# Kernel tuning notes

Measured on AMD Instinct MI355X. Metric: run time of the kernel, lower is better.

Reference implementation:

```python
import jax, jax.numpy as jnp
import numpy as np

H = 4      # num_heads
C = 64     # attention_num_c
C_Z = 128  # num_in_c (pair rep channels)
C_T = 64   # num_in_c_kv (template pair channels)


def setup_inputs() -> dict:
    key = jax.random.key(0)
    ks = jax.random.split(key, 7)
    B, T, R = 1, 4, 384
    z2d = jax.random.normal(ks[0], (B, R, R, C_Z), dtype=jnp.float32)
    t2d = jax.random.normal(ks[1], (B, T, R, R, C_T), dtype=jnp.float32)
    s = 0.02
    Wq = jax.random.normal(ks[2], (C_Z, H * C), dtype=jnp.float32) * s
    Wk = jax.random.normal(ks[3], (C_T, H * C), dtype=jnp.float32) * s
    Wv = jax.random.normal(ks[4], (C_T, H * C), dtype=jnp.float32) * s
    Wo = jax.random.normal(ks[5], (H * C, C_Z), dtype=jnp.float32) * s
    bo = jax.random.normal(ks[6], (C_Z,), dtype=jnp.float32) * s
    return {"z2d": z2d, "t2d": t2d, "Wq": Wq, "Wk": Wk, "Wv": Wv, "Wo": Wo, "bo": bo}


def reference(z2d, t2d, Wq, Wk, Wv, Wo, bo):
    B, R = z2d.shape[0], z2d.shape[-2]
    T = t2d.shape[1]
    P = R * R  # residue-pair axis
    # query: one query per residue pair
    zq = z2d.reshape(B, P, 1, C_Z)
    # templates become the key/value axis per residue pair
    tkv = jnp.transpose(t2d, (0, 2, 3, 1, 4)).reshape(B, P, T, C_T)
    q = (zq @ Wq).reshape(B, P, 1, H, C) * (C ** -0.5)
    k = (tkv @ Wk).reshape(B, P, T, H, C)
    v = (tkv @ Wv).reshape(B, P, T, H, C)
    logits = jnp.einsum('bpqhc,bpkhc->bphqk', q, k)  # [B,P,H,1,T]
    weights = jax.nn.softmax(logits, axis=-1)
    weighted_avg = jnp.einsum('bphqk,bpkhc->bpqhc', weights, v)  # [B,P,1,H,C]
    out = weighted_avg.reshape(B, P, 1, H * C) @ Wo + bo
    return out.reshape(B, R, R, C_Z)
```

## Files before the change

### kernel.cpp

```cpp
#include <hip/hip_runtime.h>


#define R_    384
#define P_    (R_ * R_)
#define PB    32
#define NPB   256
#define NT_   18

typedef __attribute__((ext_vector_type(8))) short  short8;
typedef __attribute__((ext_vector_type(4))) float  f32x4;

union S8U { short8 s8; unsigned u[4]; };

__device__ __forceinline__ unsigned short f2bf(float f) {
  unsigned u = __float_as_uint(f);
  unsigned r = ((u >> 16) & 1u) + 0x7FFFu;
  return (unsigned short)((u + r) >> 16);
}
__device__ __forceinline__ float bf2f(unsigned short s) {
  return __uint_as_float(((unsigned)s) << 16);
}
__device__ __forceinline__ unsigned cvtpk(float lo, float hi) {
  unsigned d;
  asm("v_cvt_pk_bf16_f32 %0, %1, %2" : "=v"(d) : "v"(lo), "v"(hi));
  return d;
}
__device__ __forceinline__ int swz(int p, int c) {
  return p * 256 + ((((c >> 3) ^ (p & 31)) << 3) | (c & 7));
}
#define SB() __builtin_amdgcn_sched_barrier(0)
#define BAR() do { \
    asm volatile("s_waitcnt lgkmcnt(0)\ns_barrier" ::: "memory"); \
    SB(); \
  } while (0)

__global__ void prep_kernel(const float* __restrict__ Wq, const float* __restrict__ Wk,
                            const float* __restrict__ Wv, const float* __restrict__ Wo,
                            unsigned short* __restrict__ AbarT,
                            unsigned short* __restrict__ MbarT) {
  int tid = blockIdx.x * blockDim.x + threadIdx.x;
  if (tid < 256 * 128) {
    int n = tid >> 7, i = tid & 127;
    int h = n >> 6, j = n & 63;
    const float* wq = Wq + i * 256 + h * 64;
    const float* wk = Wk + j * 256 + h * 64;
    float acc = 0.f;
#pragma unroll 8
    for (int c = 0; c < 64; ++c) acc += wq[c] * wk[c];
    AbarT[n * 128 + i] = f2bf(acc * 0.125f);
  } else {
    int t2 = tid - 256 * 128;
    int o = t2 >> 8, k = t2 & 255;
    int h = k >> 6, j = k & 63;
    const float* wv = Wv + j * 256 + h * 64;
    const float* wo = Wo + (h * 64) * 128 + o;
    float acc = 0.f;
#pragma unroll 8
    for (int c = 0; c < 64; ++c) acc += wv[c] * wo[c * 128];
    MbarT[o * 256 + k] = f2bf(acc);
  }
}

__global__ __launch_bounds__(512, 2) void attn_kernel(
    const float* __restrict__ z2d, const float* __restrict__ t2d,
    const unsigned short* __restrict__ AbarT, const unsigned short* __restrict__ MbarT,
    const float* __restrict__ bo, float* __restrict__ out) {
  extern __shared__ char smem[];
  unsigned short* sAbar = (unsigned short*)smem;
  unsigned short* sG    = (unsigned short*)(smem + 65536);

  const int tid  = threadIdx.x;
  const int wv_  = tid >> 6;
  const int lane = tid & 63;
  const int l = lane & 15;
  const int q = lane >> 4;
  const int mt = wv_ & 1;
  const int ng = wv_ >> 1;

  const int ap = tid >> 4, asub = tid & 15;
  const int ah = asub >> 2, au = asub & 3;
  const int aoG0 = swz(ap, ah * 64 + au * 16);
  const int aoG1 = swz(ap, ah * 64 + au * 16 + 8);

  const int p2g = mt * 16 + l;

#pragma unroll
  for (int k2 = 0; k2 < 8; ++k2) {
    int id = k2 * 512 + tid, n = id >> 4, blk = id & 15;
    short8 v = *(const short8*)(AbarT + n * 128 + blk * 8);
    *(short8*)(sAbar + n * 128 + ((blk ^ (n & 15)) << 3)) = v;
  }
  short8 mb0[8], mb1[8];
#pragma unroll
  for (int kk = 0; kk < 8; ++kk) {
    mb0[kk] = *(const short8*)(MbarT + (size_t)(ng * 32 + l) * 256 + kk * 32 + q * 8);
    mb1[kk] = *(const short8*)(MbarT + (size_t)(ng * 32 + 16 + l) * 256 + kk * 32 + q * 8);
  }
  const float bo0 = bo[ng * 32 + l];
  const float bo1 = bo[ng * 32 + 16 + l];
  SB();
  float4 kt[4][4];
  {
    const float* kb = t2d + ((size_t)blockIdx.x * PB + ap) * 64 + au * 16;
#pragma unroll
    for (int t = 0; t < 4; ++t)
#pragma unroll
      for (int j = 0; j < 4; ++j)
        kt[t][j] = *(const float4*)(kb + (size_t)t * (P_ * 64) + 4 * j);
  }
  SB();
  float4 zb[8];
  {
    const float* zr = z2d + ((size_t)blockIdx.x * PB + mt * 16 + l) * 128;
#pragma unroll
    for (int kk = 0; kk < 4; ++kk) {
      zb[2 * kk]     = *(const float4*)(zr + kk * 32 + q * 8);
      zb[2 * kk + 1] = *(const float4*)(zr + kk * 32 + q * 8 + 4);
    }
  }
  BAR();

#pragma unroll 1
  for (int k = 0; k < NT_; ++k) {
    const int sl = k & 1;
    const size_t P0  = (size_t)(blockIdx.x + (size_t)k * NPB) * PB;
    const size_t P0n = P0 + (size_t)NPB * PB;

    if (k > 0) {
      const unsigned short* sGp = sG + (sl ^ 1) * 8192;
      f32x4 a20 = f32x4{0.f, 0.f, 0.f, 0.f};
      f32x4 a21 = f32x4{0.f, 0.f, 0.f, 0.f};
#pragma unroll
      for (int kk = 0; kk < 8; ++kk) {
        short8 af2 = *(const short8*)(sGp + p2g * 256 + (((kk * 4 + q) ^ p2g) << 3));
        a20 = __builtin_amdgcn_mfma_f32_16x16x32_bf16(af2, mb0[kk], a20, 0, 0, 0);
        a21 = __builtin_amdgcn_mfma_f32_16x16x32_bf16(af2, mb1[kk], a21, 0, 0, 0);
      }
      const size_t rb = (P0 - (size_t)NPB * PB + (size_t)(mt * 16 + q * 4)) * 128;
#pragma unroll
      for (int r = 0; r < 4; ++r) {
        out[rb + r * 128 + ng * 32 + l]      = a20[r] + bo0;
        out[rb + r * 128 + ng * 32 + 16 + l] = a21[r] + bo1;
      }
    }
    SB();
    {
      f32x4 a1[4];
#pragma unroll
      for (int i = 0; i < 4; ++i) a1[i] = f32x4{0.f, 0.f, 0.f, 0.f};
#pragma unroll
      for (int kk = 0; kk < 4; ++kk) {
        S8U af;
        af.u[0] = cvtpk(zb[2 * kk].x,     zb[2 * kk].y);
        af.u[1] = cvtpk(zb[2 * kk].z,     zb[2 * kk].w);
        af.u[2] = cvtpk(zb[2 * kk + 1].x, zb[2 * kk + 1].y);
        af.u[3] = cvtpk(zb[2 * kk + 1].z, zb[2 * kk + 1].w);
#pragma unroll
        for (int i = 0; i < 4; ++i) {
          const int n = (ng * 4 + i) * 16 + l;
          short8 bf = *(const short8*)(sAbar + n * 128 + (((kk * 4 + q) ^ l) << 3));
          a1[i] = __builtin_amdgcn_mfma_f32_16x16x32_bf16(af.s8, bf, a1[i], 0, 0, 0);
        }
      }
      unsigned short* sGc = sG + sl * 8192;
#pragma unroll
      for (int i = 0; i < 4; ++i) {
        const int c = (ng * 4 + i) * 16 + l;
#pragma unroll
        for (int r = 0; r < 4; ++r)
          sGc[swz(mt * 16 + q * 4 + r, c)] = f2bf(a1[i][r]);
      }
    }
    SB();
    if (k + 1 < NT_) {
      const float* zr = z2d + (P0n + (size_t)(mt * 16 + l)) * 128;
#pragma unroll
      for (int kk = 0; kk < 4; ++kk) {
        zb[2 * kk]     = *(const float4*)(zr + kk * 32 + q * 8);
        zb[2 * kk + 1] = *(const float4*)(zr + kk * 32 + q * 8 + 4);
      }
    }
    SB();
    BAR();

    {
      unsigned short* sGc = sG + sl * 8192;
      short8 g0 = *(const short8*)(sGc + aoG0);
      short8 g1 = *(const short8*)(sGc + aoG1);
      float lg0 = 0.f, lg1 = 0.f, lg2 = 0.f, lg3 = 0.f;
#pragma unroll
      for (int j = 0; j < 4; ++j) {
        const float ga = bf2f((unsigned short)((j < 2) ? g0[4 * j]     : g1[4 * (j - 2)]));
        const float gb = bf2f((unsigned short)((j < 2) ? g0[4 * j + 1] : g1[4 * (j - 2) + 1]));
        const float gc = bf2f((unsigned short)((j < 2) ? g0[4 * j + 2] : g1[4 * (j - 2) + 2]));
        const float gd = bf2f((unsigned short)((j < 2) ? g0[4 * j + 3] : g1[4 * (j - 2) + 3]));
        lg0 += ga * kt[0][j].x + gb * kt[0][j].y + gc * kt[0][j].z + gd * kt[0][j].w;
        lg1 += ga * kt[1][j].x + gb * kt[1][j].y + gc * kt[1][j].z + gd * kt[1][j].w;
        lg2 += ga * kt[2][j].x + gb * kt[2][j].y + gc * kt[2][j].z + gd * kt[2][j].w;
        lg3 += ga * kt[3][j].x + gb * kt[3][j].y + gc * kt[3][j].z + gd * kt[3][j].w;
      }
      lg0 += __shfl_xor(lg0, 1); lg0 += __shfl_xor(lg0, 2);
      lg1 += __shfl_xor(lg1, 1); lg1 += __shfl_xor(lg1, 2);
      lg2 += __shfl_xor(lg2, 1); lg2 += __shfl_xor(lg2, 2);
      lg3 += __shfl_xor(lg3, 1); lg3 += __shfl_xor(lg3, 2);
      const float mx = fmaxf(fmaxf(lg0, lg1), fmaxf(lg2, lg3));
      float e0 = __expf(lg0 - mx), e1 = __expf(lg1 - mx);
      float e2 = __expf(lg2 - mx), e3 = __expf(lg3 - mx);
      const float inv = 1.f / (e0 + e1 + e2 + e3);
      e0 *= inv; e1 *= inv; e2 *= inv; e3 *= inv;
#pragma unroll
      for (int j = 0; j < 4; ++j) {
        float s0 = e0 * kt[0][j].x + e1 * kt[1][j].x + e2 * kt[2][j].x + e3 * kt[3][j].x;
        float s1 = e0 * kt[0][j].y + e1 * kt[1][j].y + e2 * kt[2][j].y + e3 * kt[3][j].y;
        float s2 = e0 * kt[0][j].z + e1 * kt[1][j].z + e2 * kt[2][j].z + e3 * kt[3][j].z;
        float s3 = e0 * kt[0][j].w + e1 * kt[1][j].w + e2 * kt[2][j].w + e3 * kt[3][j].w;
        uint2 w2; w2.x = cvtpk(s0, s1); w2.y = cvtpk(s2, s3);
        *(uint2*)(sGc + swz(ap, ah * 64 + au * 16 + 4 * j)) = w2;
      }
    }
    SB();
    if (k + 1 < NT_) {
      const float* kb = t2d + (P0n + ap) * 64 + au * 16;
#pragma unroll
      for (int t = 0; t < 4; ++t)
#pragma unroll
        for (int j = 0; j < 4; ++j)
          kt[t][j] = *(const float4*)(kb + (size_t)t * (P_ * 64) + 4 * j);
    }
    SB();
    BAR();
  }

  {
    const unsigned short* sGp = sG + 8192;
    f32x4 a20 = f32x4{0.f, 0.f, 0.f, 0.f};
    f32x4 a21 = f32x4{0.f, 0.f, 0.f, 0.f};
#pragma unroll
    for (int kk = 0; kk < 8; ++kk) {
      short8 af2 = *(const short8*)(sGp + p2g * 256 + (((kk * 4 + q) ^ p2g) << 3));
      a20 = __builtin_amdgcn_mfma_f32_16x16x32_bf16(af2, mb0[kk], a20, 0, 0, 0);
      a21 = __builtin_amdgcn_mfma_f32_16x16x32_bf16(af2, mb1[kk], a21, 0, 0, 0);
    }
    const size_t rb = ((size_t)(blockIdx.x + (size_t)(NT_ - 1) * NPB) * PB
                       + (size_t)(mt * 16 + q * 4)) * 128;
#pragma unroll
    for (int r = 0; r < 4; ++r) {
      out[rb + r * 128 + ng * 32 + l]      = a20[r] + bo0;
      out[rb + r * 128 + ng * 32 + 16 + l] = a21[r] + bo1;
    }
  }
}

extern "C" void kernel_launch(void* const* d_in, const int* in_sizes, int n_in,
                              void* d_out, int out_size, void* d_ws, size_t ws_size,
                              hipStream_t stream) {
  const float* z2d = (const float*)d_in[0];
  const float* t2d = (const float*)d_in[1];
  const float* Wq  = (const float*)d_in[2];
  const float* Wk  = (const float*)d_in[3];
  const float* Wv  = (const float*)d_in[4];
  const float* Wo  = (const float*)d_in[5];
  const float* bo  = (const float*)d_in[6];

  unsigned short* AbarT = (unsigned short*)d_ws;
  unsigned short* MbarT = AbarT + 256 * 128;
  float* out = (float*)d_out;

  static bool attr_set = false;
  if (!attr_set) {
    (void)hipFuncSetAttribute((const void*)attn_kernel,
                              hipFuncAttributeMaxDynamicSharedMemorySize, 98304);
    attr_set = true;
  }

  hipLaunchKernelGGL(prep_kernel, dim3(256), dim3(256), 0, stream,
                     Wq, Wk, Wv, Wo, AbarT, MbarT);
  hipLaunchKernelGGL(attn_kernel, dim3(NPB), dim3(512), 98304, stream,
                     z2d, t2d, AbarT, MbarT, bo, out);
}
```

Measured before the change: 310.7 us.

## Double pair tile per block to 1024 threads and drop register prefetch

Each block now handles 64 residue pairs per iteration with 1024 threads (16 waves), which halves the number of loop iterations. The register-level prefetch of the next z2d and t2d tiles is removed, and those loads are now issued at the top of the iteration that uses them. The aim is more waves per block to hide memory latency through occupancy rather than software prefetch, at the cost of load latency now sitting on the critical path, larger shared memory (128 KB) and fewer registers per thread.

```diff
diff --git a/kernel.cpp b/kernel.cpp
--- a/kernel.cpp
+++ b/kernel.cpp
@@ -3,9 +3,9 @@
 
 #define R_    384
 #define P_    (R_ * R_)
-#define PB    32
+#define PB    64
 #define NPB   256
-#define NT_   18
+#define NT_   9
 
 typedef __attribute__((ext_vector_type(8))) short  short8;
 typedef __attribute__((ext_vector_type(4))) float  f32x4;
@@ -61,7 +61,7 @@
   }
 }
 
-__global__ __launch_bounds__(512, 2) void attn_kernel(
+__global__ __launch_bounds__(1024, 4) void attn_kernel(
     const float* __restrict__ z2d, const float* __restrict__ t2d,
     const unsigned short* __restrict__ AbarT, const unsigned short* __restrict__ MbarT,
     const float* __restrict__ bo, float* __restrict__ out) {
@@ -74,19 +74,20 @@
   const int lane = tid & 63;
   const int l = lane & 15;
   const int q = lane >> 4;
-  const int mt = wv_ & 1;
-  const int ng = wv_ >> 1;
-
-  const int ap = tid >> 4, asub = tid & 15;
-  const int ah = asub >> 2, au = asub & 3;
+  const int mt = wv_ & 3;
+  const int ng = wv_ >> 2;
+
+  const int ap = tid >> 4;
+  const int ah = (tid >> 2) & 3;
+  const int au = tid & 3;
   const int aoG0 = swz(ap, ah * 64 + au * 16);
   const int aoG1 = swz(ap, ah * 64 + au * 16 + 8);
 
   const int p2g = mt * 16 + l;
 
 #pragma unroll
-  for (int k2 = 0; k2 < 8; ++k2) {
-    int id = k2 * 512 + tid, n = id >> 4, blk = id & 15;
+  for (int k2 = 0; k2 < 4; ++k2) {
+    int id = k2 * 1024 + tid, n = id >> 4, blk = id & 15;
     short8 v = *(const short8*)(AbarT + n * 128 + blk * 8);
     *(short8*)(sAbar + n * 128 + ((blk ^ (n & 15)) << 3)) = v;
   }
@@ -98,41 +99,30 @@
   }
   const float bo0 = bo[ng * 32 + l];
   const float bo1 = bo[ng * 32 + 16 + l];
-  SB();
-  float4 kt[4][4];
-  {
-    const float* kb = t2d + ((size_t)blockIdx.x * PB + ap) * 64 + au * 16;
-#pragma unroll
-    for (int t = 0; t < 4; ++t)
-#pragma unroll
-      for (int j = 0; j < 4; ++j)
-        kt[t][j] = *(const float4*)(kb + (size_t)t * (P_ * 64) + 4 * j);
-  }
-  SB();
-  float4 zb[8];
-  {
-    const float* zr = z2d + ((size_t)blockIdx.x * PB + mt * 16 + l) * 128;
-#pragma unroll
-    for (int kk = 0; kk < 4; ++kk) {
-      zb[2 * kk]     = *(const float4*)(zr + kk * 32 + q * 8);
-      zb[2 * kk + 1] = *(const float4*)(zr + kk * 32 + q * 8 + 4);
-    }
-  }
   BAR();
 
 #pragma unroll 1
   for (int k = 0; k < NT_; ++k) {
     const int sl = k & 1;
-    const size_t P0  = (size_t)(blockIdx.x + (size_t)k * NPB) * PB;
-    const size_t P0n = P0 + (size_t)NPB * PB;
-
+    const size_t P0 = (size_t)(blockIdx.x + (size_t)k * NPB) * PB;
+
+    float4 zb[8];
+    {
+      const float* zr = z2d + (P0 + (size_t)(mt * 16 + l)) * 128;
+#pragma unroll
+      for (int kk = 0; kk < 4; ++kk) {
+        zb[2 * kk]     = *(const float4*)(zr + kk * 32 + q * 8);
+        zb[2 * kk + 1] = *(const float4*)(zr + kk * 32 + q * 8 + 4);
+      }
+    }
+    SB();
     if (k > 0) {
-      const unsigned short* sGp = sG + (sl ^ 1) * 8192;
+      const unsigned short* sGp = sG + (sl ^ 1) * 16384;
       f32x4 a20 = f32x4{0.f, 0.f, 0.f, 0.f};
       f32x4 a21 = f32x4{0.f, 0.f, 0.f, 0.f};
 #pragma unroll
       for (int kk = 0; kk < 8; ++kk) {
-        short8 af2 = *(const short8*)(sGp + p2g * 256 + (((kk * 4 + q) ^ p2g) << 3));
+        short8 af2 = *(const short8*)(sGp + p2g * 256 + (((kk * 4 + q) ^ (p2g & 31)) << 3));
         a20 = __builtin_amdgcn_mfma_f32_16x16x32_bf16(af2, mb0[kk], a20, 0, 0, 0);
         a21 = __builtin_amdgcn_mfma_f32_16x16x32_bf16(af2, mb1[kk], a21, 0, 0, 0);
       }
@@ -162,7 +152,7 @@
           a1[i] = __builtin_amdgcn_mfma_f32_16x16x32_bf16(af.s8, bf, a1[i], 0, 0, 0);
         }
       }
-      unsigned short* sGc = sG + sl * 8192;
+      unsigned short* sGc = sG + sl * 16384;
 #pragma unroll
       for (int i = 0; i < 4; ++i) {
         const int c = (ng * 4 + i) * 16 + l;
@@ -172,19 +162,20 @@
       }
     }
     SB();
-    if (k + 1 < NT_) {
-      const float* zr = z2d + (P0n + (size_t)(mt * 16 + l)) * 128;
-#pragma unroll
-      for (int kk = 0; kk < 4; ++kk) {
-        zb[2 * kk]     = *(const float4*)(zr + kk * 32 + q * 8);
-        zb[2 * kk + 1] = *(const float4*)(zr + kk * 32 + q * 8 + 4);
-      }
+    float4 kt[4][4];
+    {
+      const float* kb = t2d + (P0 + ap) * 64 + au * 16;
+#pragma unroll
+      for (int t = 0; t < 4; ++t)
+#pragma unroll
+        for (int j = 0; j < 4; ++j)
+          kt[t][j] = *(const float4*)(kb + (size_t)t * (P_ * 64) + 4 * j);
     }
     SB();
     BAR();
 
     {
-      unsigned short* sGc = sG + sl * 8192;
+      unsigned short* sGc = sG + sl * 16384;
       short8 g0 = *(const short8*)(sGc + aoG0);
       short8 g1 = *(const short8*)(sGc + aoG1);
       float lg0 = 0.f, lg1 = 0.f, lg2 = 0.f, lg3 = 0.f;
@@ -219,25 +210,16 @@
       }
     }
     SB();
-    if (k + 1 < NT_) {
-      const float* kb = t2d + (P0n + ap) * 64 + au * 16;
-#pragma unroll
-      for (int t = 0; t < 4; ++t)
-#pragma unroll
-        for (int j = 0; j < 4; ++j)
-          kt[t][j] = *(const float4*)(kb + (size_t)t * (P_ * 64) + 4 * j);
-    }
-    SB();
     BAR();
   }
 
   {
-    const unsigned short* sGp = sG + 8192;
+    const unsigned short* sGp = sG + ((NT_ - 1) & 1) * 16384;
     f32x4 a20 = f32x4{0.f, 0.f, 0.f, 0.f};
     f32x4 a21 = f32x4{0.f, 0.f, 0.f, 0.f};
 #pragma unroll
     for (int kk = 0; kk < 8; ++kk) {
-      short8 af2 = *(const short8*)(sGp + p2g * 256 + (((kk * 4 + q) ^ p2g) << 3));
+      short8 af2 = *(const short8*)(sGp + p2g * 256 + (((kk * 4 + q) ^ (p2g & 31)) << 3));
       a20 = __builtin_amdgcn_mfma_f32_16x16x32_bf16(af2, mb0[kk], a20, 0, 0, 0);
       a21 = __builtin_amdgcn_mfma_f32_16x16x32_bf16(af2, mb1[kk], a21, 0, 0, 0);
     }
@@ -269,12 +251,12 @@
   static bool attr_set = false;
   if (!attr_set) {
     (void)hipFuncSetAttribute((const void*)attn_kernel,
-                              hipFuncAttributeMaxDynamicSharedMemorySize, 98304);
+                              hipFuncAttributeMaxDynamicSharedMemorySize, 131072);
     attr_set = true;
   }
 
   hipLaunchKernelGGL(prep_kernel, dim3(256), dim3(256), 0, stream,
                      Wq, Wk, Wv, Wo, AbarT, MbarT);
-  hipLaunchKernelGGL(attn_kernel, dim3(NPB), dim3(512), 98304, stream,
+  hipLaunchKernelGGL(attn_kernel, dim3(NPB), dim3(1024), 131072, stream,
                      z2d, t2d, AbarT, MbarT, bo, out);
 }
```

After: 392.1 us. +26.2%, slower.
